# Kernel tuning notes

Measured on AMD Instinct MI355X. Metric: run time of the kernel, lower is better.

## Reference

```python
import jax, jax.numpy as jnp
import numpy as np

N_NODES = 100000
N_EDGES = 1600000
IN_DIM, HID, OUT_DIM = 512, 32, 40


def setup_inputs() -> dict:
    key = jax.random.key(0)
    ks = jax.random.split(key, 6)
    x = jax.random.normal(ks[0], (N_NODES, IN_DIM), dtype=jnp.float32)
    edge_index = jax.random.randint(ks[1], (2, N_EDGES), 0, N_NODES, dtype=jnp.int64)
    # Glorot-ish init for the linear weights
    W1 = jax.random.normal(ks[2], (IN_DIM, HID), dtype=jnp.float32) / np.sqrt(IN_DIM)
    b1 = jnp.zeros((HID,), dtype=jnp.float32)
    W2 = jax.random.normal(ks[3], (HID, OUT_DIM), dtype=jnp.float32) / np.sqrt(HID)
    b2 = jnp.zeros((OUT_DIM,), dtype=jnp.float32)
    return {"x": x, "edge_index": edge_index, "W1": W1, "b1": b1, "W2": W2, "b2": b2}


def gcn_conv(x, W, b, src, dst, n_nodes):
    """PyG GCNConv: h = D^{-1/2} (A + I) D^{-1/2} (x W) + b."""
    h = x @ W  # linear transform first (reduces edge-level traffic)
    # add self-loops
    loop = jnp.arange(n_nodes, dtype=src.dtype)
    s = jnp.concatenate([src, loop])
    d = jnp.concatenate([dst, loop])
    # symmetric normalization from in-degree (including self-loops)
    deg = jax.ops.segment_sum(jnp.ones_like(d, dtype=h.dtype), d, num_segments=n_nodes)
    dinv = jnp.where(deg > 0, jax.lax.rsqrt(deg), 0.0)
    norm = dinv[s] * dinv[d]  # [E+N]
    msg = h[s] * norm[:, None]  # gather + scale
    out = jax.ops.segment_sum(msg, d, num_segments=n_nodes)  # scatter-add
    return out + b


def reference(x, edge_index, W1, b1, W2, b2):
    src, dst = edge_index[0], edge_index[1]
    n = x.shape[0]
    h = jax.nn.relu(gcn_conv(x, W1, b1, src, dst, n))
    # dropout is identity in eval mode (reference runs in eval)
    out = gcn_conv(h, W2, b2, src, dst, n)
    return out
```

## Files before the change

kernel.cpp:

```cpp
#include <hip/hip_runtime.h>
#include <hip/hip_bf16.h>

#define N_IN 512
#define HID 32
#define OUTD 40
#define NWIN 8

typedef __attribute__((ext_vector_type(8))) short bf16x8;
typedef __attribute__((ext_vector_type(4))) float f32x4;


__global__ void k_zero_i(int* p, int n) {
    int i = blockIdx.x * blockDim.x + threadIdx.x;
    if (i < n) p[i] = 0;
}

__global__ void k_count(const int* __restrict__ dst, int* cnt, int e) {
    int i = (blockIdx.x * blockDim.x + threadIdx.x) * 4;
    if (i + 3 < e) {
        int4 d4 = *(const int4*)&dst[i];
        atomicAdd(&cnt[d4.x], 1);
        atomicAdd(&cnt[d4.y], 1);
        atomicAdd(&cnt[d4.z], 1);
        atomicAdd(&cnt[d4.w], 1);
    } else {
        for (int k = i; k < e; k++) atomicAdd(&cnt[dst[k]], 1);
    }
}

__global__ void k_fill_pad(int* __restrict__ csr, int tot4, int n,
                           float* __restrict__ g1, float* __restrict__ p)
{
    int i = blockIdx.x * blockDim.x + threadIdx.x;
    if (i < tot4) {
        int4 v = make_int4(n, n, n, n);
        *(int4*)&csr[(size_t)i * 4] = v;
    }
    if (blockIdx.x == 0) {
        float4 z = make_float4(0.f, 0.f, 0.f, 0.f);
        if (threadIdx.x < 8)
            *(float4*)&g1[(size_t)n * HID + threadIdx.x * 4] = z;
        else if (threadIdx.x < 16)
            *(float4*)&p[(size_t)n * HID + (threadIdx.x - 8) * 4] = z;
    }
}

__global__ __launch_bounds__(256) void k_scan1(const int* __restrict__ cnt,
                                               int* __restrict__ offs,
                                               int* __restrict__ bsums, int n)
{
    __shared__ int sm[256];
    int t = threadIdx.x;
    int base = blockIdx.x * 1024 + t * 4;
    int a0 = (base + 0 < n) ? cnt[base + 0] : 0;
    int a1 = (base + 1 < n) ? cnt[base + 1] : 0;
    int a2 = (base + 2 < n) ? cnt[base + 2] : 0;
    int a3 = (base + 3 < n) ? cnt[base + 3] : 0;
    int d0 = (a0 + 15) & ~15;
    int d1 = (a1 + 15) & ~15;
    int d2 = (a2 + 15) & ~15;
    int d3 = (a3 + 15) & ~15;
    int s = d0 + d1 + d2 + d3;
    sm[t] = s;
    __syncthreads();
#pragma unroll
    for (int off = 1; off < 256; off <<= 1) {
        int v = (t >= off) ? sm[t - off] : 0;
        __syncthreads();
        sm[t] += v;
        __syncthreads();
    }
    int excl = sm[t] - s;
    if (base + 0 < n) offs[base + 0] = excl;
    if (base + 1 < n) offs[base + 1] = excl + d0;
    if (base + 2 < n) offs[base + 2] = excl + d0 + d1;
    if (base + 3 < n) offs[base + 3] = excl + d0 + d1 + d2;
    if (t == 255) bsums[blockIdx.x] = sm[255];
}

__global__ __launch_bounds__(256) void k_scan2(int* bsums, int nb)
{
    __shared__ int sm[256];
    int t = threadIdx.x;
    int s = (t < nb) ? bsums[t] : 0;
    sm[t] = s;
    __syncthreads();
#pragma unroll
    for (int off = 1; off < 256; off <<= 1) {
        int v = (t >= off) ? sm[t - off] : 0;
        __syncthreads();
        sm[t] += v;
        __syncthreads();
    }
    if (t < nb) bsums[t] = sm[t] - s;
}

__global__ void k_scan3(int* __restrict__ offs, int* __restrict__ cursor,
                        const int* __restrict__ bsums, const int* __restrict__ cnt,
                        float* __restrict__ dinv, int n)
{
    int i = blockIdx.x * blockDim.x + threadIdx.x;
    if (i >= n) return;
    int o = offs[i] + bsums[i >> 10];
    offs[i] = o;
    cursor[i] = o;
    dinv[i] = rsqrtf((float)(cnt[i] + 1));
}

__global__ void k_fill_win(const int* __restrict__ src, const int* __restrict__ dst,
                           int* cursor, int* __restrict__ csr, int e, int wlo, int whi)
{
    int i = (blockIdx.x * blockDim.x + threadIdx.x) * 4;
    if (i >= e) return;
    if (i + 3 < e) {
        int4 d4 = *(const int4*)&dst[i];
        int dd[4] = {d4.x, d4.y, d4.z, d4.w};
#pragma unroll
        for (int k = 0; k < 4; k++) {
            int d = dd[k];
            if (d >= wlo && d < whi) {
                int p = atomicAdd(&cursor[d], 1);
                csr[p] = src[i + k];
            }
        }
    } else {
        for (int k = i; k < e; k++) {
            int d = dst[k];
            if (d >= wlo && d < whi) {
                int p = atomicAdd(&cursor[d], 1);
                csr[p] = src[k];
            }
        }
    }
}

__global__ void k_convw(const float* __restrict__ W, unsigned short* __restrict__ wfh,
                        unsigned short* __restrict__ wfl)
{
    int idx = blockIdx.x * blockDim.x + threadIdx.x;
    int j     = idx & 7;
    int lane  = (idx >> 3) & 63;
    int ntile = (idx >> 9) & 1;
    int kstep = idx >> 10;
    int k    = kstep * 32 + (lane >> 4) * 8 + j;
    int ncol = ntile * 16 + (lane & 15);
    float v = W[k * HID + ncol];
    unsigned u = __builtin_bit_cast(unsigned, v);
    unsigned short h = (unsigned short)(u >> 16);
    float hv = __builtin_bit_cast(float, u & 0xFFFF0000u);
    float rem = v - hv;
    unsigned ur = __builtin_bit_cast(unsigned, rem);
    ur += 0x7FFF + ((ur >> 16) & 1);
    wfh[idx] = h;
    wfl[idx] = (unsigned short)(ur >> 16);
}

__global__ __launch_bounds__(256) void k_gemm1(
    const float* __restrict__ x,
    const unsigned short* __restrict__ wfh, const unsigned short* __restrict__ wfl,
    const float* __restrict__ dinv, float* __restrict__ g1, int n)
{
    const int t    = threadIdx.x;
    const int lane = t & 63;
    const int wave = t >> 6;
    const int m    = lane & 15;
    const int quad = lane >> 4;
    const int row0 = blockIdx.x * 64 + wave * 16;

    int arow = row0 + m;
    if (arow >= n) arow = n - 1;
    const float* xp = x + (size_t)arow * N_IN + quad * 8;

    f32x4 acc0 = {0.f, 0.f, 0.f, 0.f};
    f32x4 acc1 = {0.f, 0.f, 0.f, 0.f};

    for (int ks = 0; ks < 16; ks++) {
        float4 xa = *(const float4*)(xp + ks * 32);
        float4 xb = *(const float4*)(xp + ks * 32 + 4);
        float xe[8] = {xa.x, xa.y, xa.z, xa.w, xb.x, xb.y, xb.z, xb.w};
        bf16x8 ah, al;
#pragma unroll
        for (int j = 0; j < 8; j++) {
            unsigned u = __builtin_bit_cast(unsigned, xe[j]);
            ah[j] = (short)(u >> 16);
            float hv = __builtin_bit_cast(float, u & 0xFFFF0000u);
            float rem = xe[j] - hv;
            unsigned ur = __builtin_bit_cast(unsigned, rem);
            ur += 0x7FFF + ((ur >> 16) & 1);
            al[j] = (short)(ur >> 16);
        }
        bf16x8 bh0 = *(const bf16x8*)(wfh + ((size_t)(ks * 2 + 0) * 64 + lane) * 8);
        bf16x8 bh1 = *(const bf16x8*)(wfh + ((size_t)(ks * 2 + 1) * 64 + lane) * 8);
        bf16x8 bl0 = *(const bf16x8*)(wfl + ((size_t)(ks * 2 + 0) * 64 + lane) * 8);
        bf16x8 bl1 = *(const bf16x8*)(wfl + ((size_t)(ks * 2 + 1) * 64 + lane) * 8);

        acc0 = __builtin_amdgcn_mfma_f32_16x16x32_bf16(ah, bh0, acc0, 0, 0, 0);
        acc0 = __builtin_amdgcn_mfma_f32_16x16x32_bf16(al, bh0, acc0, 0, 0, 0);
        acc0 = __builtin_amdgcn_mfma_f32_16x16x32_bf16(ah, bl0, acc0, 0, 0, 0);
        acc1 = __builtin_amdgcn_mfma_f32_16x16x32_bf16(ah, bh1, acc1, 0, 0, 0);
        acc1 = __builtin_amdgcn_mfma_f32_16x16x32_bf16(al, bh1, acc1, 0, 0, 0);
        acc1 = __builtin_amdgcn_mfma_f32_16x16x32_bf16(ah, bl1, acc1, 0, 0, 0);
    }

#pragma unroll
    for (int r = 0; r < 4; r++) {
        int row = row0 + quad * 4 + r;
        if (row < n) {
            float dv = dinv[row];
            g1[(size_t)row * HID + m]      = acc0[r] * dv;
            g1[(size_t)row * HID + 16 + m] = acc1[r] * dv;
        }
    }
}


__global__ void k_agg1(const int* __restrict__ csr, const int* __restrict__ offs,
                       const int* __restrict__ cnt, const float* __restrict__ g,
                       const float* __restrict__ dinv, const float* __restrict__ b1,
                       float* __restrict__ p, int n)
{
    int gid = blockIdx.x * blockDim.x + threadIdx.x;
    int r  = gid >> 4;
    int sl = gid & 15;
    if (r >= n) return;
    int s0 = offs[r];
    int dp = (cnt[r] + 15) & ~15;
    int half = sl >> 3;
    int c = sl & 7;
    const float* gc = g + c * 4;
    float4 acc = make_float4(0.f, 0.f, 0.f, 0.f);
    if (half == 0) acc = *(const float4*)&gc[(size_t)r * HID];
    for (int b = 0; b < dp; b += 16) {
        int s = csr[s0 + b + sl];
#pragma unroll
        for (int jj = 0; jj < 8; jj++) {
            int sj = __shfl(s, jj + (half << 3), 16);
            float4 v = *(const float4*)&gc[(size_t)sj * HID];
            acc.x += v.x; acc.y += v.y; acc.z += v.z; acc.w += v.w;
        }
    }
    float4 o;
    o.x = __shfl(acc.x, sl ^ 8, 16);
    o.y = __shfl(acc.y, sl ^ 8, 16);
    o.z = __shfl(acc.z, sl ^ 8, 16);
    o.w = __shfl(acc.w, sl ^ 8, 16);
    if (half == 0) {
        float dv = dinv[r];
        float4 bv = *(const float4*)&b1[c * 4];
        float4 hp;
        hp.x = dv * fmaxf((acc.x + o.x) * dv + bv.x, 0.f);
        hp.y = dv * fmaxf((acc.y + o.y) * dv + bv.y, 0.f);
        hp.z = dv * fmaxf((acc.z + o.z) * dv + bv.z, 0.f);
        hp.w = dv * fmaxf((acc.w + o.w) * dv + bv.w, 0.f);
        *(float4*)&p[(size_t)r * HID + c * 4] = hp;
    }
}

__global__ void k_agg2(const int* __restrict__ csr, const int* __restrict__ offs,
                       const int* __restrict__ cnt, const float* __restrict__ g,
                       const float* __restrict__ dinv, float* __restrict__ acc2, int n)
{
    int gid = blockIdx.x * blockDim.x + threadIdx.x;
    int r  = gid >> 4;
    int sl = gid & 15;
    if (r >= n) return;
    int s0 = offs[r];
    int dp = (cnt[r] + 15) & ~15;
    int half = sl >> 3;
    int c = sl & 7;
    const float* gc = g + c * 4;
    float4 acc = make_float4(0.f, 0.f, 0.f, 0.f);
    if (half == 0) acc = *(const float4*)&gc[(size_t)r * HID];
    for (int b = 0; b < dp; b += 16) {
        int s = csr[s0 + b + sl];
#pragma unroll
        for (int jj = 0; jj < 8; jj++) {
            int sj = __shfl(s, jj + (half << 3), 16);
            float4 v = *(const float4*)&gc[(size_t)sj * HID];
            acc.x += v.x; acc.y += v.y; acc.z += v.z; acc.w += v.w;
        }
    }
    float4 o;
    o.x = __shfl(acc.x, sl ^ 8, 16);
    o.y = __shfl(acc.y, sl ^ 8, 16);
    o.z = __shfl(acc.z, sl ^ 8, 16);
    o.w = __shfl(acc.w, sl ^ 8, 16);
    if (half == 0) {
        float dv = dinv[r];
        float4 v;
        v.x = (acc.x + o.x) * dv;
        v.y = (acc.y + o.y) * dv;
        v.z = (acc.z + o.z) * dv;
        v.w = (acc.w + o.w) * dv;
        *(float4*)&acc2[(size_t)r * HID + c * 4] = v;
    }
}

__global__ void k_out(const float* __restrict__ acc2, const float* __restrict__ W2,
                      const float* __restrict__ b2, float* __restrict__ out, int n)
{
    int r = blockIdx.x * blockDim.x + threadIdx.x;
    if (r >= n) return;
    float h[HID];
#pragma unroll
    for (int k4 = 0; k4 < HID / 4; k4++) {
        float4 v = *(const float4*)&acc2[(size_t)r * HID + k4 * 4];
        h[k4 * 4 + 0] = v.x;
        h[k4 * 4 + 1] = v.y;
        h[k4 * 4 + 2] = v.z;
        h[k4 * 4 + 3] = v.w;
    }
    float o[OUTD];
#pragma unroll
    for (int c = 0; c < OUTD; c++) o[c] = b2[c];
#pragma unroll
    for (int k = 0; k < HID; k++) {
        float hv = h[k];
        const float* wr = &W2[k * OUTD];
#pragma unroll
        for (int c = 0; c < OUTD; c++) o[c] += hv * wr[c];
    }
    float* gp = &out[(size_t)r * OUTD];
#pragma unroll
    for (int c4 = 0; c4 < OUTD / 4; c4++) {
        float4 v;
        v.x = o[c4 * 4 + 0];
        v.y = o[c4 * 4 + 1];
        v.z = o[c4 * 4 + 2];
        v.w = o[c4 * 4 + 3];
        *(float4*)&gp[c4 * 4] = v;
    }
}

extern "C" void kernel_launch(void* const* d_in, const int* in_sizes, int n_in,
                              void* d_out, int out_size, void* d_ws, size_t ws_size,
                              hipStream_t stream)
{
    const float* x  = (const float*)d_in[0];
    const int*   ei = (const int*)d_in[1];
    const float* W1 = (const float*)d_in[2];
    const float* b1 = (const float*)d_in[3];
    const float* W2 = (const float*)d_in[4];
    const float* b2 = (const float*)d_in[5];
    float* out = (float*)d_out;

    const int n = in_sizes[0] / N_IN;
    const int e = in_sizes[1] / 2;
    const int* src = ei;
    const int* dst = ei + e;

    const int csr_cap = e + 16 * n;

    char* w = (char*)d_ws;
    float* dinv   = (float*)w;            w += sizeof(float) * (size_t)((n + 3) & ~3);
    float* g1     = (float*)w;            w += sizeof(float) * (size_t)(n + 1) * HID;
    float* p      = (float*)w;            w += sizeof(float) * (size_t)(n + 1) * HID;
    float* acc2   = (float*)w;            w += sizeof(float) * (size_t)n * HID;
    int*   cnt    = (int*)w;              w += sizeof(int) * (size_t)((n + 3) & ~3);
    int*   offs   = (int*)w;              w += sizeof(int) * (size_t)((n + 3) & ~3);
    int*   cursor = (int*)w;              w += sizeof(int) * (size_t)((n + 3) & ~3);
    int*   bsums  = (int*)w;              w += sizeof(int) * 1024;
    unsigned short* wfh = (unsigned short*)w;  w += sizeof(unsigned short) * 16384;
    unsigned short* wfl = (unsigned short*)w;  w += sizeof(unsigned short) * 16384;
    int*   csr    = (int*)w;              w += sizeof(int) * (size_t)((csr_cap + 3) & ~3);

    const int nb = (n + 1023) / 1024;
    const int ec = (e + 3) / 4;
    const int tot4 = (csr_cap + 3) / 4;

    k_zero_i<<<(n + 255) / 256, 256, 0, stream>>>(cnt, n);
    k_count<<<(ec + 255) / 256, 256, 0, stream>>>(dst, cnt, e);
    k_fill_pad<<<(tot4 + 255) / 256, 256, 0, stream>>>(csr, tot4, n, g1, p);
    k_scan1<<<nb, 256, 0, stream>>>(cnt, offs, bsums, n);
    k_scan2<<<1, 256, 0, stream>>>(bsums, nb);
    k_scan3<<<(n + 255) / 256, 256, 0, stream>>>(offs, cursor, bsums, cnt, dinv, n);

    for (int wdx = 0; wdx < NWIN; wdx++) {
        int wlo = (int)((long)n * wdx / NWIN);
        int whi = (int)((long)n * (wdx + 1) / NWIN);
        k_fill_win<<<(ec + 255) / 256, 256, 0, stream>>>(src, dst, cursor, csr, e, wlo, whi);
    }

    k_convw<<<64, 256, 0, stream>>>(W1, wfh, wfl);

    k_gemm1<<<(n + 63) / 64, 256, 0, stream>>>(x, wfh, wfl, dinv, g1, n);

    int t16 = n * 16;
    k_agg1<<<(t16 + 255) / 256, 256, 0, stream>>>(csr, offs, cnt, g1, dinv, b1, p, n);
    k_agg2<<<(t16 + 255) / 256, 256, 0, stream>>>(csr, offs, cnt, p, dinv, acc2, n);

    k_out<<<(n + 255) / 256, 256, 0, stream>>>(acc2, W2, b2, out, n);
}
```

Measured before the change: 578.4 us.

## Fuse zero/pad init, single-pass CSR fill, fuse agg2 with output projection

Merges the count-zeroing and CSR padding kernels into one init kernel. Replaces the eight windowed CSR fill passes with a single pass that also loads src vectorised, trading destination locality for fewer reads of the edge list. Fuses the second aggregation with the W2 projection, using lane shuffles so the acc2 intermediate buffer and its extra kernel disappear. Unwindowed scatter may have poorer cache behaviour for atomics and CSR writes.

```diff
diff --git a/kernel.cpp b/kernel.cpp
--- a/kernel.cpp
+++ b/kernel.cpp
@@ -4,15 +4,31 @@
 #define N_IN 512
 #define HID 32
 #define OUTD 40
-#define NWIN 8
 
 typedef __attribute__((ext_vector_type(8))) short bf16x8;
 typedef __attribute__((ext_vector_type(4))) float f32x4;
 
 
-__global__ void k_zero_i(int* p, int n) {
+__global__ void k_init(int* __restrict__ csr, int tot4, int n4, int n,
+                       float* __restrict__ g1, float* __restrict__ p,
+                       int* __restrict__ cnt)
+{
     int i = blockIdx.x * blockDim.x + threadIdx.x;
-    if (i < n) p[i] = 0;
+    if (i < tot4) {
+        int4 v = make_int4(n, n, n, n);
+        *(int4*)&csr[(size_t)i * 4] = v;
+    }
+    if (i < n4) {
+        int4 z4 = make_int4(0, 0, 0, 0);
+        *(int4*)&cnt[(size_t)i * 4] = z4;
+    }
+    if (blockIdx.x == 0) {
+        float4 z = make_float4(0.f, 0.f, 0.f, 0.f);
+        if (threadIdx.x < 8)
+            *(float4*)&g1[(size_t)n * HID + threadIdx.x * 4] = z;
+        else if (threadIdx.x < 16)
+            *(float4*)&p[(size_t)n * HID + (threadIdx.x - 8) * 4] = z;
+    }
 }
 
 __global__ void k_count(const int* __restrict__ dst, int* cnt, int e) {
@@ -25,23 +41,6 @@
         atomicAdd(&cnt[d4.w], 1);
     } else {
         for (int k = i; k < e; k++) atomicAdd(&cnt[dst[k]], 1);
-    }
-}
-
-__global__ void k_fill_pad(int* __restrict__ csr, int tot4, int n,
-                           float* __restrict__ g1, float* __restrict__ p)
-{
-    int i = blockIdx.x * blockDim.x + threadIdx.x;
-    if (i < tot4) {
-        int4 v = make_int4(n, n, n, n);
-        *(int4*)&csr[(size_t)i * 4] = v;
-    }
-    if (blockIdx.x == 0) {
-        float4 z = make_float4(0.f, 0.f, 0.f, 0.f);
-        if (threadIdx.x < 8)
-            *(float4*)&g1[(size_t)n * HID + threadIdx.x * 4] = z;
-        else if (threadIdx.x < 16)
-            *(float4*)&p[(size_t)n * HID + (threadIdx.x - 8) * 4] = z;
     }
 }
 
@@ -107,29 +106,25 @@
     dinv[i] = rsqrtf((float)(cnt[i] + 1));
 }
 
-__global__ void k_fill_win(const int* __restrict__ src, const int* __restrict__ dst,
-                           int* cursor, int* __restrict__ csr, int e, int wlo, int whi)
+__global__ void k_fill(const int* __restrict__ src, const int* __restrict__ dst,
+                       int* cursor, int* __restrict__ csr, int e)
 {
     int i = (blockIdx.x * blockDim.x + threadIdx.x) * 4;
     if (i >= e) return;
     if (i + 3 < e) {
         int4 d4 = *(const int4*)&dst[i];
+        int4 s4 = *(const int4*)&src[i];
         int dd[4] = {d4.x, d4.y, d4.z, d4.w};
+        int ss[4] = {s4.x, s4.y, s4.z, s4.w};
 #pragma unroll
         for (int k = 0; k < 4; k++) {
-            int d = dd[k];
-            if (d >= wlo && d < whi) {
-                int p = atomicAdd(&cursor[d], 1);
-                csr[p] = src[i + k];
-            }
+            int p = atomicAdd(&cursor[dd[k]], 1);
+            csr[p] = ss[k];
         }
     } else {
         for (int k = i; k < e; k++) {
-            int d = dst[k];
-            if (d >= wlo && d < whi) {
-                int p = atomicAdd(&cursor[d], 1);
-                csr[p] = src[k];
-            }
+            int p = atomicAdd(&cursor[dst[k]], 1);
+            csr[p] = src[k];
         }
     }
 }
@@ -256,9 +251,10 @@
     }
 }
 
-__global__ void k_agg2(const int* __restrict__ csr, const int* __restrict__ offs,
-                       const int* __restrict__ cnt, const float* __restrict__ g,
-                       const float* __restrict__ dinv, float* __restrict__ acc2, int n)
+__global__ void k_agg2_out(const int* __restrict__ csr, const int* __restrict__ offs,
+                           const int* __restrict__ cnt, const float* __restrict__ g,
+                           const float* __restrict__ dinv, const float* __restrict__ W2,
+                           const float* __restrict__ b2, float* __restrict__ out, int n)
 {
     int gid = blockIdx.x * blockDim.x + threadIdx.x;
     int r  = gid >> 4;
@@ -285,51 +281,30 @@
     o.y = __shfl(acc.y, sl ^ 8, 16);
     o.z = __shfl(acc.z, sl ^ 8, 16);
     o.w = __shfl(acc.w, sl ^ 8, 16);
-    if (half == 0) {
-        float dv = dinv[r];
-        float4 v;
-        v.x = (acc.x + o.x) * dv;
-        v.y = (acc.y + o.y) * dv;
-        v.z = (acc.z + o.z) * dv;
-        v.w = (acc.w + o.w) * dv;
-        *(float4*)&acc2[(size_t)r * HID + c * 4] = v;
-    }
-}
-
-__global__ void k_out(const float* __restrict__ acc2, const float* __restrict__ W2,
-                      const float* __restrict__ b2, float* __restrict__ out, int n)
-{
-    int r = blockIdx.x * blockDim.x + threadIdx.x;
-    if (r >= n) return;
-    float h[HID];
-#pragma unroll
-    for (int k4 = 0; k4 < HID / 4; k4++) {
-        float4 v = *(const float4*)&acc2[(size_t)r * HID + k4 * 4];
-        h[k4 * 4 + 0] = v.x;
-        h[k4 * 4 + 1] = v.y;
-        h[k4 * 4 + 2] = v.z;
-        h[k4 * 4 + 3] = v.w;
-    }
-    float o[OUTD];
-#pragma unroll
-    for (int c = 0; c < OUTD; c++) o[c] = b2[c];
-#pragma unroll
-    for (int k = 0; k < HID; k++) {
-        float hv = h[k];
-        const float* wr = &W2[k * OUTD];
-#pragma unroll
-        for (int c = 0; c < OUTD; c++) o[c] += hv * wr[c];
-    }
-    float* gp = &out[(size_t)r * OUTD];
-#pragma unroll
-    for (int c4 = 0; c4 < OUTD / 4; c4++) {
-        float4 v;
-        v.x = o[c4 * 4 + 0];
-        v.y = o[c4 * 4 + 1];
-        v.z = o[c4 * 4 + 2];
-        v.w = o[c4 * 4 + 3];
-        *(float4*)&gp[c4 * 4] = v;
-    }
+    float dv = dinv[r];
+    float h0 = (acc.x + o.x) * dv;
+    float h1 = (acc.y + o.y) * dv;
+    float h2 = (acc.z + o.z) * dv;
+    float h3 = (acc.w + o.w) * dv;
+
+    int oc = (sl < 10) ? sl * 4 : 0;
+    float4 ov = *(const float4*)&b2[oc];
+#pragma unroll
+    for (int k4 = 0; k4 < 8; k4++) {
+        float a0 = __shfl(h0, k4, 16);
+        float a1 = __shfl(h1, k4, 16);
+        float a2 = __shfl(h2, k4, 16);
+        float a3 = __shfl(h3, k4, 16);
+        float4 w0 = *(const float4*)&W2[(4 * k4 + 0) * OUTD + oc];
+        float4 w1 = *(const float4*)&W2[(4 * k4 + 1) * OUTD + oc];
+        float4 w2 = *(const float4*)&W2[(4 * k4 + 2) * OUTD + oc];
+        float4 w3 = *(const float4*)&W2[(4 * k4 + 3) * OUTD + oc];
+        ov.x += a0 * w0.x + a1 * w1.x + a2 * w2.x + a3 * w3.x;
+        ov.y += a0 * w0.y + a1 * w1.y + a2 * w2.y + a3 * w3.y;
+        ov.z += a0 * w0.z + a1 * w1.z + a2 * w2.z + a3 * w3.z;
+        ov.w += a0 * w0.w + a1 * w1.w + a2 * w2.w + a3 * w3.w;
+    }
+    if (sl < 10) *(float4*)&out[(size_t)r * OUTD + sl * 4] = ov;
 }
 
 extern "C" void kernel_launch(void* const* d_in, const int* in_sizes, int n_in,
@@ -355,7 +330,6 @@
     float* dinv   = (float*)w;            w += sizeof(float) * (size_t)((n + 3) & ~3);
     float* g1     = (float*)w;            w += sizeof(float) * (size_t)(n + 1) * HID;
     float* p      = (float*)w;            w += sizeof(float) * (size_t)(n + 1) * HID;
-    float* acc2   = (float*)w;            w += sizeof(float) * (size_t)n * HID;
     int*   cnt    = (int*)w;              w += sizeof(int) * (size_t)((n + 3) & ~3);
     int*   offs   = (int*)w;              w += sizeof(int) * (size_t)((n + 3) & ~3);
     int*   cursor = (int*)w;              w += sizeof(int) * (size_t)((n + 3) & ~3);
@@ -366,20 +340,16 @@
 
     const int nb = (n + 1023) / 1024;
     const int ec = (e + 3) / 4;
+    const int n4 = (n + 3) / 4;
     const int tot4 = (csr_cap + 3) / 4;
-
-    k_zero_i<<<(n + 255) / 256, 256, 0, stream>>>(cnt, n);
+    const int initN = (tot4 > n4) ? tot4 : n4;
+
+    k_init<<<(initN + 255) / 256, 256, 0, stream>>>(csr, tot4, n4, n, g1, p, cnt);
     k_count<<<(ec + 255) / 256, 256, 0, stream>>>(dst, cnt, e);
-    k_fill_pad<<<(tot4 + 255) / 256, 256, 0, stream>>>(csr, tot4, n, g1, p);
     k_scan1<<<nb, 256, 0, stream>>>(cnt, offs, bsums, n);
     k_scan2<<<1, 256, 0, stream>>>(bsums, nb);
     k_scan3<<<(n + 255) / 256, 256, 0, stream>>>(offs, cursor, bsums, cnt, dinv, n);
-
-    for (int wdx = 0; wdx < NWIN; wdx++) {
-        int wlo = (int)((long)n * wdx / NWIN);
-        int whi = (int)((long)n * (wdx + 1) / NWIN);
-        k_fill_win<<<(ec + 255) / 256, 256, 0, stream>>>(src, dst, cursor, csr, e, wlo, whi);
-    }
+    k_fill<<<(ec + 255) / 256, 256, 0, stream>>>(src, dst, cursor, csr, e);
 
     k_convw<<<64, 256, 0, stream>>>(W1, wfh, wfl);
 
@@ -387,7 +357,5 @@
 
     int t16 = n * 16;
     k_agg1<<<(t16 + 255) / 256, 256, 0, stream>>>(csr, offs, cnt, g1, dinv, b1, p, n);
-    k_agg2<<<(t16 + 255) / 256, 256, 0, stream>>>(csr, offs, cnt, p, dinv, acc2, n);
-
-    k_out<<<(n + 255) / 256, 256, 0, stream>>>(acc2, W2, b2, out, n);
-}
+    k_agg2_out<<<(t16 + 255) / 256, 256, 0, stream>>>(csr, offs, cnt, p, dinv, W2, b2, out, n);
+}
```

Measured after the change: 596.1 us. 1.03x slower.
